# Kernel tuning notes

Measured on AMD Instinct MI355X. Metric: run time of the kernel, lower is better.

## Reference

```python
import math
import jax, jax.numpy as jnp
import numpy as np

V_VOCAB, D_MODEL, N_LAYERS, N_HEADS, D_K = 256, 1024, 16, 16, 64
BATCH, SEQ = 2, 2048


def setup_inputs() -> dict:
    key = jax.random.key(0)
    ks = jax.random.split(key, 7)
    s = 0.02
    return {
        "input_ids": jax.random.randint(ks[0], (BATCH, SEQ), 0, V_VOCAB),
        "emb": jax.random.normal(ks[1], (V_VOCAB, D_MODEL), jnp.float32) * s,
        # per-layer projection weights stored [in, out] (torch Linear weight transposed)
        "Wq": jax.random.normal(ks[2], (N_LAYERS, D_MODEL, N_HEADS * D_K), jnp.float32) * s,
        "Wk": jax.random.normal(ks[3], (N_LAYERS, D_MODEL, N_HEADS * D_K), jnp.float32) * s,
        "Wv": jax.random.normal(ks[4], (N_LAYERS, D_MODEL, N_HEADS * D_K), jnp.float32) * s,
        "Wo": jax.random.normal(ks[5], (N_LAYERS, N_HEADS * D_K, D_MODEL), jnp.float32) * s,
        "Wout": jax.random.normal(ks[6], (D_MODEL, V_VOCAB), jnp.float32) * s,
    }


def reference(input_ids, emb, Wq, Wk, Wv, Wo, Wout):
    B, S = input_ids.shape
    # TextInput: prepend bos=0 column, then embed -> [B, n, D]
    ids = jnp.pad(input_ids, ((0, 0), (1, 0)), constant_values=0)
    x0 = emb[ids]
    n = S + 1
    # Mask('causal'): 0 on lower-triangle, -inf above (1 - 1/tril(ones))
    causal = jnp.where(jnp.tril(jnp.ones((n, n), bool)), 0.0, -jnp.inf).astype(x0.dtype)
    scale = 1.0 / math.sqrt(D_K)

    def split_heads(y):  # [B,n,H*dk] -> [B,H,n,dk]
        return y.reshape(B, n, N_HEADS, D_K).transpose(0, 2, 1, 3)

    @jax.checkpoint
    def layer(x, w):
        wq, wk, wv, wo = w
        Q = split_heads(x @ wq)
        K = split_heads(x @ wk)
        Vh = split_heads(x @ wv)
        scores = jnp.einsum('bhqd,bhkd->bhqk', Q * scale, K) + causal
        A = jax.nn.softmax(scores, axis=-1)
        o = jnp.einsum('bhqk,bhkd->bhqd', A, Vh)
        o = o.transpose(0, 2, 1, 3).reshape(B, n, N_HEADS * D_K)
        xn = x + o @ wo
        return xn, xn

    _, xs = jax.lax.scan(layer, x0, (Wq, Wk, Wv, Wo))
    xs_all = jnp.concatenate([x0[None], xs], axis=0)  # [L+1, B, n, D]
    # TextOutput: linear (no bias) then softmax over vocab
    probs = jax.nn.softmax(xs_all @ Wout, axis=-1)  # [L+1, B, n, V]
    return probs
```

## Files before the change

### kernel.cpp

```cpp
#include <hip/hip_runtime.h>
#include <math.h>


#define NSEQ 2049
#define NTOK 4098
#define DM   1024
#define VOC  256

typedef unsigned short u16;
typedef __bf16 bf16x8 __attribute__((ext_vector_type(8)));
typedef float f32x4 __attribute__((ext_vector_type(4)));

__device__ __forceinline__ u16 f2b(float f) {
  union { float f; unsigned u; } v; v.f = f;
  unsigned r = v.u + 0x7FFFu + ((v.u >> 16) & 1u);
  return (u16)(r >> 16);
}

__device__ __forceinline__ void stage16(const u16* g, u16* l) {
  __builtin_amdgcn_global_load_lds(
      (__attribute__((address_space(1))) void*)(void*)g,
      (__attribute__((address_space(3))) void*)l, 16, 0, 0);
}

__device__ __forceinline__ f32x4 mfma16(bf16x8 a, bf16x8 b, f32x4 c) {
  return __builtin_amdgcn_mfma_f32_16x16x32_bf16(a, b, c, 0, 0, 0);
}

__global__ __launch_bounds__(256) void k_embed(const int* __restrict__ ids,
    const float* __restrict__ emb, float* __restrict__ x, u16* __restrict__ xb) {
  int row = blockIdx.x;
  int b = row / NSEQ, t = row - b * NSEQ;
  int id = (t == 0) ? 0 : ids[b * (NSEQ - 1) + (t - 1)];
  float4 v = ((const float4*)(emb + (size_t)id * DM))[threadIdx.x];
  ((float4*)(x + (size_t)row * DM))[threadIdx.x] = v;
  ushort4 o; o.x = f2b(v.x); o.y = f2b(v.y); o.z = f2b(v.z); o.w = f2b(v.w);
  *(ushort4*)(xb + (size_t)row * DM + threadIdx.x * 4) = o;
}

__device__ __forceinline__ void txp64(const float* __restrict__ src,
    u16* __restrict__ dst, int C, int R, int r0, int c0) {
  __shared__ float t[64][68];
  const int tid = threadIdx.x;
  const int lr = tid >> 4, lc = (tid & 15) * 4;
#pragma unroll
  for (int p = 0; p < 4; ++p)
    *(float4*)&t[lr + 16 * p][lc] =
        *(const float4*)(src + (size_t)(r0 + lr + 16 * p) * C + c0 + lc);
  __syncthreads();
  const int oc = tid >> 2, q = tid & 3;
#pragma unroll
  for (int pass = 0; pass < 2; ++pass) {
    union { u16 us[8]; uint4 v; } ob;
#pragma unroll
    for (int i = 0; i < 8; ++i) ob.us[i] = f2b(t[pass * 32 + q * 8 + i][oc]);
    *(uint4*)(dst + (size_t)(c0 + oc) * R + r0 + pass * 32 + q * 8) = ob.v;
  }
}

__global__ __launch_bounds__(256) void k_transpose_all(const float* __restrict__ Wq,
    const float* __restrict__ Wk, const float* __restrict__ Wv,
    const float* __restrict__ Wo, u16* __restrict__ WT) {
  const int z = blockIdx.z, layer = z >> 2, mat = z & 3;
  const float* src = ((mat == 0) ? Wq : (mat == 1) ? Wk : (mat == 2) ? Wv : Wo)
                     + (size_t)layer * 1048576;
  u16* dst = WT + (size_t)z * 1048576;
  txp64(src, dst, 1024, 1024, blockIdx.y * 64, blockIdx.x * 64);
}

__global__ __launch_bounds__(256) void k_transpose4(const float* __restrict__ Wq,
    const float* __restrict__ Wk, const float* __restrict__ Wv,
    const float* __restrict__ Wo, size_t loff, u16* __restrict__ WT) {
  const int z = blockIdx.z;
  const float* src = ((z == 0) ? Wq : (z == 1) ? Wk : (z == 2) ? Wv : Wo) + loff;
  u16* dst = WT + (size_t)z * 1048576;
  txp64(src, dst, 1024, 1024, blockIdx.y * 64, blockIdx.x * 64);
}

__global__ __launch_bounds__(256) void k_transpose_gen(const float* __restrict__ src,
    u16* __restrict__ dst, int R, int C) {
  txp64(src, dst, C, R, blockIdx.y * 64, blockIdx.x * 64);
}

__global__ __launch_bounds__(256) void k_gemm_qkv(const u16* __restrict__ xb,
    const u16* __restrict__ WT, u16* __restrict__ Qb, u16* __restrict__ Kb,
    u16* __restrict__ Vt) {
  const int z = blockIdx.z;
  const u16* Ap; const u16* Bp; int Am, Bn, m0, n0;
  if (z < 2) { Ap = xb; Bp = WT + (size_t)z * 1048576; Am = NTOK; Bn = DM;
               m0 = blockIdx.x * 128; n0 = blockIdx.y * 128; }
  else       { Ap = WT + (size_t)2 * 1048576; Bp = xb; Am = DM; Bn = NTOK;
               m0 = blockIdx.y * 128; n0 = blockIdx.x * 128; }
  __shared__ __align__(16) u16 As[128 * 32], Bs[128 * 32];
  const int tid = threadIdx.x, w = tid >> 6, l = tid & 63;
  const int lo = l & 15, hi = l >> 4;
  const int wr = (w >> 1) * 64, wc = (w & 1) * 64;
  const int srow = w * 32 + (l >> 2), scol = (l & 3) * 8;
  u16* ldsA = As + w * 1024 + l * 8;
  u16* ldsB = Bs + w * 1024 + l * 8;
  f32x4 acc[4][4];
#pragma unroll
  for (int i = 0; i < 4; ++i)
#pragma unroll
    for (int j = 0; j < 4; ++j) acc[i][j] = f32x4{0.f, 0.f, 0.f, 0.f};

  for (int k0 = 0; k0 < 1024; k0 += 32) {
    __syncthreads();
#pragma unroll
    for (int c = 0; c < 2; ++c) {
      int ra = m0 + srow + c * 16; ra = ra < Am ? ra : Am - 1;
      stage16(Ap + (size_t)ra * 1024 + k0 + scol, ldsA + c * 512);
      int rb = n0 + srow + c * 16; rb = rb < Bn ? rb : Bn - 1;
      stage16(Bp + (size_t)rb * 1024 + k0 + scol, ldsB + c * 512);
    }
    __syncthreads();
    bf16x8 av[4], bv[4];
#pragma unroll
    for (int i = 0; i < 4; ++i)
      av[i] = *(const bf16x8*)(As + (wr + 16 * i + lo) * 32 + hi * 8);
#pragma unroll
    for (int j = 0; j < 4; ++j)
      bv[j] = *(const bf16x8*)(Bs + (wc + 16 * j + lo) * 32 + hi * 8);
#pragma unroll
    for (int i = 0; i < 4; ++i)
#pragma unroll
      for (int j = 0; j < 4; ++j) acc[i][j] = mfma16(av[i], bv[j], acc[i][j]);
  }
  if (z < 2) {
    u16* dst = (z == 0) ? Qb : Kb;
    const float sc = (z == 0) ? 0.125f : 1.0f;
#pragma unroll
    for (int j = 0; j < 4; ++j) {
      int col = n0 + wc + 16 * j + lo, hh = col >> 6, dd = col & 63;
#pragma unroll
      for (int i = 0; i < 4; ++i)
#pragma unroll
        for (int r = 0; r < 4; ++r) {
          int tok = m0 + wr + 16 * i + hi * 4 + r;
          if (tok < NTOK) {
            int bb = tok >= NSEQ, tt = tok - bb * NSEQ;
            dst[((size_t)(bb * 16 + hh) * NSEQ + tt) * 64 + dd] =
                f2b(acc[i][j][r] * sc);
          }
        }
    }
  } else {
#pragma unroll
    for (int j = 0; j < 4; ++j) {
      int tok = n0 + wc + 16 * j + lo;
      if (tok < NTOK) {
        int bb = tok >= NSEQ, tt = tok - bb * NSEQ;
#pragma unroll
        for (int i = 0; i < 4; ++i)
#pragma unroll
          for (int r = 0; r < 4; ++r) {
            int dg = m0 + wr + 16 * i + hi * 4 + r;
            Vt[(size_t)(bb * 1024 + dg) * 2112 + tt] = f2b(acc[i][j][r]);
          }
      }
    }
  }
}

__global__ __launch_bounds__(256) void k_gemm_out(const u16* __restrict__ Ob,
    const u16* __restrict__ WTo, float* __restrict__ x, u16* __restrict__ xb) {
  const int m0 = blockIdx.x * 128, n0 = blockIdx.y * 128;
  __shared__ __align__(16) u16 As[128 * 32], Bs[128 * 32];
  const int tid = threadIdx.x, w = tid >> 6, l = tid & 63;
  const int lo = l & 15, hi = l >> 4;
  const int wr = (w >> 1) * 64, wc = (w & 1) * 64;
  const int srow = w * 32 + (l >> 2), scol = (l & 3) * 8;
  u16* ldsA = As + w * 1024 + l * 8;
  u16* ldsB = Bs + w * 1024 + l * 8;
  f32x4 acc[4][4];
#pragma unroll
  for (int i = 0; i < 4; ++i)
#pragma unroll
    for (int j = 0; j < 4; ++j) acc[i][j] = f32x4{0.f, 0.f, 0.f, 0.f};

  for (int k0 = 0; k0 < 1024; k0 += 32) {
    __syncthreads();
#pragma unroll
    for (int c = 0; c < 2; ++c) {
      int ra = m0 + srow + c * 16; ra = ra < NTOK ? ra : NTOK - 1;
      stage16(Ob + (size_t)ra * 1024 + k0 + scol, ldsA + c * 512);
      int rb = n0 + srow + c * 16;
      stage16(WTo + (size_t)rb * 1024 + k0 + scol, ldsB + c * 512);
    }
    __syncthreads();
    bf16x8 av[4], bv[4];
#pragma unroll
    for (int i = 0; i < 4; ++i)
      av[i] = *(const bf16x8*)(As + (wr + 16 * i + lo) * 32 + hi * 8);
#pragma unroll
    for (int j = 0; j < 4; ++j)
      bv[j] = *(const bf16x8*)(Bs + (wc + 16 * j + lo) * 32 + hi * 8);
#pragma unroll
    for (int i = 0; i < 4; ++i)
#pragma unroll
      for (int j = 0; j < 4; ++j) acc[i][j] = mfma16(av[i], bv[j], acc[i][j]);
  }
#pragma unroll
  for (int i = 0; i < 4; ++i)
#pragma unroll
    for (int r = 0; r < 4; ++r) {
      int tok = m0 + wr + 16 * i + hi * 4 + r;
      if (tok < NTOK) {
#pragma unroll
        for (int j = 0; j < 4; ++j) {
          int col = n0 + wc + 16 * j + lo;
          size_t idx = (size_t)tok * DM + col;
          float v = x[idx] + acc[i][j][r];
          x[idx] = v; xb[idx] = f2b(v);
        }
      }
    }
}

__global__ __launch_bounds__(256) void k_attn(const u16* __restrict__ Q,
    const u16* __restrict__ K, const u16* __restrict__ Vt, u16* __restrict__ O) {
  const int qt = 16 - blockIdx.x, h = blockIdx.y, b = blockIdx.z;
  const int tid = threadIdx.x, w = tid >> 6, l = tid & 63;
  const int lo = l & 15, hi = l >> 4;
  const int q0 = qt * 128;
  const size_t bh = (size_t)(b * 16 + h) * NSEQ * 64;

  __shared__ __align__(16) u16 QPs[128 * 72];
  __shared__ __align__(16) u16 Ks[64 * 72], Vs[64 * 72];
  __shared__ float Ls[128];

  {
    const int r = tid >> 3, c8 = (tid & 7) * 8;
#pragma unroll
    for (int p = 0; p < 4; ++p) {
      int row = r + 32 * p;
      int gq = q0 + row; gq = gq < NSEQ ? gq : NSEQ - 1;
      *(uint4*)(QPs + row * 72 + c8) = *(const uint4*)(Q + bh + (size_t)gq * 64 + c8);
    }
  }
  __syncthreads();
  bf16x8 bq[2][2];
#pragma unroll
  for (int nq = 0; nq < 2; ++nq)
#pragma unroll
    for (int c = 0; c < 2; ++c)
      bq[nq][c] = *(const bf16x8*)(QPs + (w * 32 + nq * 16 + lo) * 72 + c * 32 + hi * 8);

  f32x4 oa[2][4];
  f32x4 la4[2];
#pragma unroll
  for (int i = 0; i < 2; ++i) {
    la4[i] = f32x4{0.f, 0.f, 0.f, 0.f};
#pragma unroll
    for (int nt = 0; nt < 4; ++nt) oa[i][nt] = f32x4{0.f, 0.f, 0.f, 0.f};
  }

  const int qstrip = q0 + w * 32;
  const int ktmax = 2 * qt + 2;
  for (int kt = 0; kt < ktmax; ++kt) {
    const int k0 = kt * 64;
    __syncthreads();
    {
      const int r = tid >> 3, c8 = (tid & 7) * 8;
#pragma unroll
      for (int p = 0; p < 2; ++p) {
        int row = r + 32 * p;
        int gk = k0 + row; gk = gk < NSEQ ? gk : NSEQ - 1;
        *(uint4*)(Ks + row * 72 + c8) = *(const uint4*)(K + bh + (size_t)gk * 64 + c8);
        *(uint4*)(Vs + row * 72 + c8) =
            *(const uint4*)(Vt + (size_t)(b * 1024 + h * 64 + row) * 2112 + k0 + c8);
      }
    }
    __syncthreads();
    if (k0 > qstrip + 31) continue;

    f32x4 st[4][2];
#pragma unroll
    for (int mk = 0; mk < 4; ++mk) {
      bf16x8 ak0 = *(const bf16x8*)(Ks + (mk * 16 + lo) * 72 + hi * 8);
      bf16x8 ak1 = *(const bf16x8*)(Ks + (mk * 16 + lo) * 72 + 32 + hi * 8);
#pragma unroll
      for (int nq = 0; nq < 2; ++nq) {
        f32x4 z = f32x4{0.f, 0.f, 0.f, 0.f};
        z = mfma16(ak0, bq[nq][0], z);
        st[mk][nq] = mfma16(ak1, bq[nq][1], z);
      }
    }
    const bool needMask = (k0 + 63 > qstrip);
#pragma unroll
    for (int mk = 0; mk < 4; ++mk)
#pragma unroll
      for (int nq = 0; nq < 2; ++nq) {
        if (needMask) {
          int query = qstrip + nq * 16 + lo;
          int keyb = k0 + mk * 16 + hi * 4;
#pragma unroll
          for (int r = 0; r < 4; ++r)
            if (keyb + r > query) st[mk][nq][r] = -INFINITY;
        }
        f32x4 e;
#pragma unroll
        for (int r = 0; r < 4; ++r) e[r] = __expf(st[mk][nq][r]);
        la4[nq] += e;
        ushort4 u; u.x = f2b(e[0]); u.y = f2b(e[1]); u.z = f2b(e[2]); u.w = f2b(e[3]);
        *(ushort4*)(QPs + (w * 32 + nq * 16 + lo) * 72 + mk * 16 + hi * 4) = u;
      }
    bf16x8 ap[2][2];
#pragma unroll
    for (int i = 0; i < 2; ++i)
#pragma unroll
      for (int c = 0; c < 2; ++c)
        ap[i][c] = *(const bf16x8*)(QPs + (w * 32 + i * 16 + lo) * 72 + c * 32 + hi * 8);
#pragma unroll
    for (int nt = 0; nt < 4; ++nt) {
      bf16x8 v0 = *(const bf16x8*)(Vs + (nt * 16 + lo) * 72 + hi * 8);
      bf16x8 v1 = *(const bf16x8*)(Vs + (nt * 16 + lo) * 72 + 32 + hi * 8);
#pragma unroll
      for (int i = 0; i < 2; ++i) {
        oa[i][nt] = mfma16(ap[i][0], v0, oa[i][nt]);
        oa[i][nt] = mfma16(ap[i][1], v1, oa[i][nt]);
      }
    }
  }
#pragma unroll
  for (int nq = 0; nq < 2; ++nq) {
    float s = la4[nq][0] + la4[nq][1] + la4[nq][2] + la4[nq][3];
    s += __shfl_xor(s, 16);
    s += __shfl_xor(s, 32);
    if (hi == 0) Ls[w * 32 + nq * 16 + lo] = 1.0f / s;
  }
#pragma unroll
  for (int i = 0; i < 2; ++i)
#pragma unroll
    for (int r = 0; r < 4; ++r) {
      int ql = w * 32 + i * 16 + hi * 4 + r;
      int q = q0 + ql;
      if (q < NSEQ) {
        float inv = Ls[ql];
#pragma unroll
        for (int nt = 0; nt < 4; ++nt)
          O[(size_t)(b * NSEQ + q) * DM + h * 64 + nt * 16 + lo] =
              f2b(oa[i][nt][r] * inv);
      }
    }
}

__global__ __launch_bounds__(256) void k_probs(const u16* __restrict__ xb,
    const u16* __restrict__ WoutT, float* __restrict__ out, int slice) {
  __shared__ __align__(16) u16 As[2][64 * 32], Bs[2][256 * 32];
  const int tid = threadIdx.x, w = tid >> 6, l = tid & 63;
  const int lo = l & 15, hi = l >> 4;
  const int m0 = blockIdx.x * 64;
  const int srow = l >> 2, scol = (l & 3) * 8;
  f32x4 acc[16];
#pragma unroll
  for (int j = 0; j < 16; ++j) acc[j] = f32x4{0.f, 0.f, 0.f, 0.f};

  int ra = m0 + w * 16 + srow; ra = ra < NTOK ? ra : NTOK - 1;
  const u16* gA = xb + (size_t)ra * 1024 + scol;

  {
    stage16(gA, As[0] + w * 512 + l * 8);
#pragma unroll
    for (int c = 0; c < 4; ++c) {
      int rb = w * 64 + c * 16 + srow;
      stage16(WoutT + (size_t)rb * 1024 + scol, Bs[0] + w * 2048 + c * 512 + l * 8);
    }
  }
  for (int t = 0; t < 32; ++t) {
    const int cur = t & 1;
    if (t < 31) {
      const int k1 = (t + 1) * 32;
      stage16(gA + k1, As[cur ^ 1] + w * 512 + l * 8);
#pragma unroll
      for (int c = 0; c < 4; ++c) {
        int rb = w * 64 + c * 16 + srow;
        stage16(WoutT + (size_t)rb * 1024 + k1 + scol,
                Bs[cur ^ 1] + w * 2048 + c * 512 + l * 8);
      }
      asm volatile("s_waitcnt vmcnt(5)" ::: "memory");
    } else {
      asm volatile("s_waitcnt vmcnt(0)" ::: "memory");
    }
    __builtin_amdgcn_s_barrier();
    bf16x8 a = *(const bf16x8*)(As[cur] + (w * 16 + lo) * 32 + hi * 8);
#pragma unroll
    for (int j = 0; j < 16; ++j) {
      bf16x8 bv = *(const bf16x8*)(Bs[cur] + (16 * j + lo) * 32 + hi * 8);
      acc[j] = mfma16(a, bv, acc[j]);
    }
    __builtin_amdgcn_s_barrier();
  }
#pragma unroll
  for (int r = 0; r < 4; ++r) {
    float sum = 0.f;
#pragma unroll
    for (int j = 0; j < 16; ++j) {
      float e = __expf(acc[j][r]);
      acc[j][r] = e; sum += e;
    }
    for (int off = 1; off < 16; off <<= 1) sum += __shfl_xor(sum, off);
    float inv = 1.0f / sum;
    int tok = m0 + w * 16 + hi * 4 + r;
    if (tok < NTOK) {
      size_t base = ((size_t)slice * NTOK + tok) * VOC;
#pragma unroll
      for (int j = 0; j < 16; ++j) out[base + 16 * j + lo] = acc[j][r] * inv;
    }
  }
}

extern "C" void kernel_launch(void* const* d_in, const int* in_sizes, int n_in,
                              void* d_out, int out_size, void* d_ws,
                              size_t ws_size, hipStream_t stream) {
  const int*   ids  = (const int*)d_in[0];
  const float* emb  = (const float*)d_in[1];
  const float* Wq   = (const float*)d_in[2];
  const float* Wk   = (const float*)d_in[3];
  const float* Wv   = (const float*)d_in[4];
  const float* Wo   = (const float*)d_in[5];
  const float* Wout = (const float*)d_in[6];
  float* out = (float*)d_out;

  char* p = (char*)d_ws;
  float* x  = (float*)p;  p += (size_t)NTOK * DM * 4;
  u16* xb   = (u16*)p;    p += (size_t)NTOK * DM * 2;
  u16* Qb   = (u16*)p;    p += (size_t)2 * 16 * NSEQ * 64 * 2;
  u16* Kb   = (u16*)p;    p += (size_t)2 * 16 * NSEQ * 64 * 2;
  u16* Vt   = (u16*)p;    p += (size_t)2 * 1024 * 2112 * 2;
  u16* Ob   = (u16*)p;    p += (size_t)NTOK * DM * 2;
  u16* WoutT = (u16*)p;   p += (size_t)1024 * 256 * 2;
  u16* WT   = (u16*)p;
  const size_t base_bytes = (size_t)(p - (char*)d_ws);
  const bool allWT = ws_size >= base_bytes + (size_t)64 * 1048576 * 2;

  k_transpose_gen<<<dim3(4, 16), 256, 0, stream>>>(Wout, WoutT, 1024, 256);
  if (allWT)
    k_transpose_all<<<dim3(16, 16, 64), 256, 0, stream>>>(Wq, Wk, Wv, Wo, WT);
  k_embed<<<NTOK, 256, 0, stream>>>(ids, emb, x, xb);
  k_probs<<<65, 256, 0, stream>>>(xb, WoutT, out, 0);

  for (int l = 0; l < 16; ++l) {
    size_t loff = (size_t)l * 1048576;
    u16* wtl = allWT ? (WT + (size_t)l * 4 * 1048576) : WT;
    if (!allWT)
      k_transpose4<<<dim3(16, 16, 4), 256, 0, stream>>>(Wq, Wk, Wv, Wo, loff, WT);
    k_gemm_qkv<<<dim3(33, 8, 3), 256, 0, stream>>>(xb, wtl, Qb, Kb, Vt);
    k_attn<<<dim3(17, 16, 2), 256, 0, stream>>>(Qb, Kb, Vt, Ob);
    k_gemm_out<<<dim3(33, 8), 256, 0, stream>>>(Ob, wtl + 3 * 1048576, x, xb);
    k_probs<<<65, 256, 0, stream>>>(xb, WoutT, out, l + 1);
  }
}
```

Baseline: 3.683 ms.

## Batch all vocab-softmax slices into one launch and loop-tile weight transposes

```diff
diff --git a/kernel.cpp b/kernel.cpp
--- a/kernel.cpp
+++ b/kernel.cpp
@@ -38,23 +38,45 @@
   *(ushort4*)(xb + (size_t)row * DM + threadIdx.x * 4) = o;
 }
 
-__device__ __forceinline__ void txp64(const float* __restrict__ src,
-    u16* __restrict__ dst, int C, int R, int r0, int c0) {
-  __shared__ float t[64][68];
+__device__ __forceinline__ void txp64v2(const float* __restrict__ src,
+    u16* __restrict__ dst, int C, int R, int r0base, int c0, int nt) {
+  __shared__ float t[64][65];
   const int tid = threadIdx.x;
   const int lr = tid >> 4, lc = (tid & 15) * 4;
+  const int oc = tid >> 2, q = tid & 3;
+  f32x4 v[4], nv[4];
+  int r0 = r0base;
 #pragma unroll
   for (int p = 0; p < 4; ++p)
-    *(float4*)&t[lr + 16 * p][lc] =
-        *(const float4*)(src + (size_t)(r0 + lr + 16 * p) * C + c0 + lc);
-  __syncthreads();
-  const int oc = tid >> 2, q = tid & 3;
-#pragma unroll
-  for (int pass = 0; pass < 2; ++pass) {
-    union { u16 us[8]; uint4 v; } ob;
-#pragma unroll
-    for (int i = 0; i < 8; ++i) ob.us[i] = f2b(t[pass * 32 + q * 8 + i][oc]);
-    *(uint4*)(dst + (size_t)(c0 + oc) * R + r0 + pass * 32 + q * 8) = ob.v;
+    v[p] = *(const f32x4*)(src + (size_t)(r0 + lr + 16 * p) * C + c0 + lc);
+  for (int it = 0; it < nt; ++it) {
+#pragma unroll
+    for (int p = 0; p < 4; ++p) {
+      const int row = lr + 16 * p;
+      t[lc + 0][row] = v[p][0]; t[lc + 1][row] = v[p][1];
+      t[lc + 2][row] = v[p][2]; t[lc + 3][row] = v[p][3];
+    }
+    if (it + 1 < nt) {
+#pragma unroll
+      for (int p = 0; p < 4; ++p)
+        nv[p] = *(const f32x4*)(src + (size_t)(r0 + 64 + lr + 16 * p) * C + c0 + lc);
+    }
+    asm volatile("s_waitcnt lgkmcnt(0)" ::: "memory");
+    __builtin_amdgcn_s_barrier();
+    union { u16 us[8]; uint4 u4; } ob;
+#pragma unroll
+    for (int pass = 0; pass < 2; ++pass) {
+#pragma unroll
+      for (int i = 0; i < 8; ++i) ob.us[i] = f2b(t[oc][pass * 32 + q * 8 + i]);
+      *(uint4*)(dst + (size_t)(c0 + oc) * R + r0 + pass * 32 + q * 8) = ob.u4;
+    }
+    r0 += 64;
+    if (it + 1 < nt) {
+      asm volatile("s_waitcnt lgkmcnt(0)" ::: "memory");
+      __builtin_amdgcn_s_barrier();
+#pragma unroll
+      for (int p = 0; p < 4; ++p) v[p] = nv[p];
+    }
   }
 }
 
@@ -65,7 +87,7 @@
   const float* src = ((mat == 0) ? Wq : (mat == 1) ? Wk : (mat == 2) ? Wv : Wo)
                      + (size_t)layer * 1048576;
   u16* dst = WT + (size_t)z * 1048576;
-  txp64(src, dst, 1024, 1024, blockIdx.y * 64, blockIdx.x * 64);
+  txp64v2(src, dst, 1024, 1024, blockIdx.y * 256, blockIdx.x * 64, 4);
 }
 
 __global__ __launch_bounds__(256) void k_transpose4(const float* __restrict__ Wq,
@@ -74,12 +96,12 @@
   const int z = blockIdx.z;
   const float* src = ((z == 0) ? Wq : (z == 1) ? Wk : (z == 2) ? Wv : Wo) + loff;
   u16* dst = WT + (size_t)z * 1048576;
-  txp64(src, dst, 1024, 1024, blockIdx.y * 64, blockIdx.x * 64);
+  txp64v2(src, dst, 1024, 1024, blockIdx.y * 256, blockIdx.x * 64, 4);
 }
 
 __global__ __launch_bounds__(256) void k_transpose_gen(const float* __restrict__ src,
     u16* __restrict__ dst, int R, int C) {
-  txp64(src, dst, C, R, blockIdx.y * 64, blockIdx.x * 64);
+  txp64v2(src, dst, C, R, blockIdx.y * 256, blockIdx.x * 64, 4);
 }
 
 __global__ __launch_bounds__(256) void k_gemm_qkv(const u16* __restrict__ xb,
@@ -346,11 +368,14 @@
 }
 
 __global__ __launch_bounds__(256) void k_probs(const u16* __restrict__ xb,
-    const u16* __restrict__ WoutT, float* __restrict__ out, int slice) {
+    const u16* __restrict__ WoutT, float* __restrict__ out, int slice0,
+    size_t sstride) {
   __shared__ __align__(16) u16 As[2][64 * 32], Bs[2][256 * 32];
   const int tid = threadIdx.x, w = tid >> 6, l = tid & 63;
   const int lo = l & 15, hi = l >> 4;
   const int m0 = blockIdx.x * 64;
+  const int slice = slice0 + blockIdx.y;
+  xb += (size_t)blockIdx.y * sstride;
   const int srow = l >> 2, scol = (l & 3) * 8;
   f32x4 acc[16];
 #pragma unroll
@@ -424,30 +449,41 @@
 
   char* p = (char*)d_ws;
   float* x  = (float*)p;  p += (size_t)NTOK * DM * 4;
-  u16* xb   = (u16*)p;    p += (size_t)NTOK * DM * 2;
   u16* Qb   = (u16*)p;    p += (size_t)2 * 16 * NSEQ * 64 * 2;
   u16* Kb   = (u16*)p;    p += (size_t)2 * 16 * NSEQ * 64 * 2;
   u16* Vt   = (u16*)p;    p += (size_t)2 * 1024 * 2112 * 2;
   u16* Ob   = (u16*)p;    p += (size_t)NTOK * DM * 2;
   u16* WoutT = (u16*)p;   p += (size_t)1024 * 256 * 2;
   u16* WT   = (u16*)p;
-  const size_t base_bytes = (size_t)(p - (char*)d_ws);
-  const bool allWT = ws_size >= base_bytes + (size_t)64 * 1048576 * 2;
-
-  k_transpose_gen<<<dim3(4, 16), 256, 0, stream>>>(Wout, WoutT, 1024, 256);
+  const size_t baseB  = (size_t)(p - (char*)d_ws);
+  const size_t sliceB = (size_t)NTOK * DM * 2;
+  const size_t sliceE = (size_t)NTOK * DM;
+  const size_t wtAll  = (size_t)64 * 1048576 * 2;
+  const size_t wt4    = (size_t)4 * 1048576 * 2;
+  const bool full  = ws_size >= baseB + wtAll + 17 * sliceB;
+  const bool allWT = full || ws_size >= baseB + wtAll + sliceB;
+  u16* xall = (u16*)((char*)WT + (allWT ? wtAll : wt4));
+
+  k_transpose_gen<<<dim3(4, 4), 256, 0, stream>>>(Wout, WoutT, 1024, 256);
   if (allWT)
-    k_transpose_all<<<dim3(16, 16, 64), 256, 0, stream>>>(Wq, Wk, Wv, Wo, WT);
-  k_embed<<<NTOK, 256, 0, stream>>>(ids, emb, x, xb);
-  k_probs<<<65, 256, 0, stream>>>(xb, WoutT, out, 0);
+    k_transpose_all<<<dim3(16, 4, 64), 256, 0, stream>>>(Wq, Wk, Wv, Wo, WT);
+  k_embed<<<NTOK, 256, 0, stream>>>(ids, emb, x, xall);
+  if (!full)
+    k_probs<<<dim3(65, 1), 256, 0, stream>>>(xall, WoutT, out, 0, 0);
 
   for (int l = 0; l < 16; ++l) {
     size_t loff = (size_t)l * 1048576;
     u16* wtl = allWT ? (WT + (size_t)l * 4 * 1048576) : WT;
+    u16* xin  = xall + (full ? (size_t)l * sliceE : 0);
+    u16* xout = xall + (full ? (size_t)(l + 1) * sliceE : 0);
     if (!allWT)
-      k_transpose4<<<dim3(16, 16, 4), 256, 0, stream>>>(Wq, Wk, Wv, Wo, loff, WT);
-    k_gemm_qkv<<<dim3(33, 8, 3), 256, 0, stream>>>(xb, wtl, Qb, Kb, Vt);
+      k_transpose4<<<dim3(16, 4, 4), 256, 0, stream>>>(Wq, Wk, Wv, Wo, loff, WT);
+    k_gemm_qkv<<<dim3(33, 8, 3), 256, 0, stream>>>(xin, wtl, Qb, Kb, Vt);
     k_attn<<<dim3(17, 16, 2), 256, 0, stream>>>(Qb, Kb, Vt, Ob);
-    k_gemm_out<<<dim3(33, 8), 256, 0, stream>>>(Ob, wtl + 3 * 1048576, x, xb);
-    k_probs<<<65, 256, 0, stream>>>(xb, WoutT, out, l + 1);
-  }
-}
+    k_gemm_out<<<dim3(33, 8), 256, 0, stream>>>(Ob, wtl + 3 * 1048576, x, xout);
+    if (!full)
+      k_probs<<<dim3(65, 1), 256, 0, stream>>>(xall, WoutT, out, l + 1, 0);
+  }
+  if (full)
+    k_probs<<<dim3(65, 17), 256, 0, stream>>>(xall, WoutT, out, 0, sliceE);
+}
```

Measured after the change: 3.667 ms. No clear change (-0.4%).
